# Kernel tuning notes

Hardware: AMD Instinct MI355X
Metric: run time of the kernel (lower is better)

## Reference

```python
import jax, jax.numpy as jnp
import numpy as np

HEADS = 4
DIM_HEAD = 32
SCALE = DIM_HEAD ** -0.5


def setup_inputs() -> dict:
    key = jax.random.key(0)
    k1, k2, k3 = jax.random.split(key, 3)
    B, C, H, W = 4, 128, 64, 64
    inner = HEADS * DIM_HEAD  # 128
    x = jax.random.normal(k1, (B, C, H, W), dtype=jnp.float32)
    # 1x1 conv weights == channel-mixing matrices [out_ch, in_ch]
    w_qkv = jax.random.normal(k2, (inner * 3, C), dtype=jnp.float32) * (C ** -0.5)
    w_proj = jax.random.normal(k3, (C, inner), dtype=jnp.float32) * (inner ** -0.5)
    b_proj = jnp.zeros((C,), dtype=jnp.float32)
    return {"x": x, "w_qkv": w_qkv, "w_proj": w_proj, "b_proj": b_proj}


def reference(x, w_qkv, w_proj, b_proj):
    b, c, h, w = x.shape
    n = h * w
    # 1x1 conv = per-pixel matmul over channels
    qkv = jnp.einsum('bchw,oc->bohw', x, w_qkv)  # [B, 3*inner, H, W]
    q, k, v = jnp.split(qkv, 3, axis=1)

    def to_heads(t):
        # [B, inner, H, W] -> [B, heads, HW, dim_head]
        return t.reshape(b, HEADS, DIM_HEAD, n).transpose(0, 1, 3, 2)

    q = to_heads(q) * SCALE
    k = to_heads(k)
    v = to_heads(v)
    # scores [B, heads, HW, HW]; softmax is max-stabilized (matches torch amax-subtract)
    scores = jnp.einsum('bhnd,bhmd->bhnm', q, k)
    attn = jax.nn.softmax(scores, axis=-1)
    out = jnp.einsum('bhnm,bhmd->bhnd', attn, v)  # [B, heads, HW, dim_head]
    out = out.transpose(0, 1, 3, 2).reshape(b, HEADS * DIM_HEAD, h, w)
    return jnp.einsum('bchw,oc->bohw', out, w_proj) + b_proj[None, :, None, None]
```

## Files before the change

kernel.cpp:

```cpp
#include <hip/hip_runtime.h>

typedef _Float16 f16;
typedef __attribute__((ext_vector_type(8))) f16 f16x8;
typedef __attribute__((ext_vector_type(4))) f16 f16x4;
typedef __attribute__((ext_vector_type(2))) __fp16 h16x2;
typedef __attribute__((ext_vector_type(4))) float floatx4;

#define NPIX 4096
#define KT   128
#define VROW 136

__global__ __launch_bounds__(256) void cvt_w(
    const float* __restrict__ wq, const float* __restrict__ wp,
    f16* __restrict__ wh, f16* __restrict__ wph)
{
    const int idx = (blockIdx.x * 256 + threadIdx.x) * 4;
    const float qs = 0.17677669529663687f * 1.4426950408889634f;
    float4 v;
    f16* dst;
    if (idx < 49152) { v = *(const float4*)(wq + idx); dst = wh + idx; }
    else             { v = *(const float4*)(wp + (idx - 49152)); dst = wph + (idx - 49152); }
    if (idx < 16384) { v.x *= qs; v.y *= qs; v.z *= qs; v.w *= qs; }
    h16x2 a = __builtin_amdgcn_cvt_pkrtz(v.x, v.y);
    h16x2 b = __builtin_amdgcn_cvt_pkrtz(v.z, v.w);
    f16x4 h; h[0] = (f16)a[0]; h[1] = (f16)a[1]; h[2] = (f16)b[0]; h[3] = (f16)b[1];
    *(f16x4*)dst = h;
}

__global__ __launch_bounds__(256) void qkv_mfma(
    const float* __restrict__ x, const f16* __restrict__ wh,
    f16* __restrict__ qh, f16* __restrict__ kh, f16* __restrict__ vth)
{
    const int tid  = threadIdx.x;
    const int wave = tid >> 6;
    const int lane = tid & 63;
    const int quad = lane >> 4;
    const int l16  = lane & 15;
    const int pbase = blockIdx.x * 64;
    const int b     = blockIdx.y;
    const int p_col = pbase + wave * 16 + l16;

    const float* xb = x + (size_t)b * 128 * NPIX;

    f16x8 xf[4];
#pragma unroll
    for (int kc = 0; kc < 4; ++kc) {
        const int c0 = kc * 32 + quad * 8;
        float e[8];
#pragma unroll
        for (int j = 0; j < 8; ++j)
            e[j] = xb[(size_t)(c0 + j) * NPIX + p_col];
#pragma unroll
        for (int j = 0; j < 4; ++j) {
            h16x2 pk = __builtin_amdgcn_cvt_pkrtz(e[2 * j], e[2 * j + 1]);
            xf[kc][2 * j] = (f16)pk[0]; xf[kc][2 * j + 1] = (f16)pk[1];
        }
    }

#pragma unroll
    for (int y = 0; y < 6; ++y) {
        floatx4 acc[4];
#pragma unroll
        for (int i = 0; i < 4; ++i) acc[i] = floatx4{0.f, 0.f, 0.f, 0.f};

        if (y < 4) {
#pragma unroll
            for (int n = 0; n < 4; ++n)
#pragma unroll
                for (int kc = 0; kc < 4; ++kc) {
                    f16x8 wf = *(const f16x8*)&wh[(size_t)(y * 64 + n * 16 + l16) * 128 + kc * 32 + quad * 8];
                    acc[n] = __builtin_amdgcn_mfma_f32_16x16x32_f16(xf[kc], wf, acc[n], 0, 0, 0);
                }
            f16* dst = (y < 2) ? qh : kh;
#pragma unroll
            for (int n = 0; n < 4; ++n) {
                const int og    = y * 64 + n * 16 + l16;
                const int local = og & 127;
                const int head  = local >> 5;
                const int d     = local & 31;
                f16* base = dst + (size_t)(b * 4 + head) * NPIX * 32;
#pragma unroll
                for (int r = 0; r < 4; ++r) {
                    const int p = pbase + wave * 16 + quad * 4 + r;
                    base[(size_t)p * 32 + d] = (f16)acc[n][r];
                }
            }
        } else {
#pragma unroll
            for (int m = 0; m < 4; ++m)
#pragma unroll
                for (int kc = 0; kc < 4; ++kc) {
                    f16x8 wf = *(const f16x8*)&wh[(size_t)(y * 64 + m * 16 + l16) * 128 + kc * 32 + quad * 8];
                    acc[m] = __builtin_amdgcn_mfma_f32_16x16x32_f16(wf, xf[kc], acc[m], 0, 0, 0);
                }
#pragma unroll
            for (int m = 0; m < 4; ++m)
#pragma unroll
                for (int r = 0; r < 4; ++r) {
                    const int ov   = (y - 4) * 64 + m * 16 + quad * 4 + r;
                    const int head = ov >> 5;
                    const int d    = ov & 31;
                    vth[((size_t)(b * 4 + head) * 32 + d) * NPIX + p_col] = (f16)acc[m][r];
                }
        }
    }
}

__global__ __launch_bounds__(256, 4) void attn_kernel(
    const f16* __restrict__ qh, const f16* __restrict__ kh,
    const f16* __restrict__ vth, f16* __restrict__ att)
{
    __shared__ f16 klds[KT * 32];
    __shared__ f16 vlds[32 * VROW];

    const int tid  = threadIdx.x;
    const int wave = tid >> 6;
    const int lane = tid & 63;
    const int quad = lane >> 4;
    const int l16  = lane & 15;

    const int n    = blockIdx.x;
    const int bh   = (n & 7) * 2 + ((n >> 3) & 1);
    const int qblk = n >> 4;
    const int qbase = qblk * 64 + wave * 16;

    const f16* kb = kh + (size_t)bh * NPIX * 32;
    const f16* vb = vth + (size_t)bh * 32 * NPIX;

    f16x8 qB = *(const f16x8*)(qh + ((size_t)bh * NPIX + qbase + l16) * 32 + quad * 8);

    floatx4 oacc[2];
    oacc[0] = floatx4{0.f, 0.f, 0.f, 0.f};
    oacc[1] = floatx4{0.f, 0.f, 0.f, 0.f};
    float lsum = 0.f;

    for (int kt = 0; kt < NPIX / KT; ++kt) {
        __syncthreads();
        {
            const int4* src = (const int4*)(kb + (size_t)kt * KT * 32);
            ((int4*)klds)[tid]       = src[tid];
            ((int4*)klds)[tid + 256] = src[tid + 256];
        }
        {
            const int r  = tid >> 3;
            const int cc = (tid & 7) * 2;
            const int4* vsrc = (const int4*)(vb + (size_t)r * NPIX + kt * KT + cc * 8);
            int4 v0 = vsrc[0], v1 = vsrc[1];
            int4* vdst = (int4*)(vlds + r * VROW + cc * 8);
            vdst[0] = v0; vdst[1] = v1;
        }
        __syncthreads();

        floatx4 st[8];
#pragma unroll
        for (int t = 0; t < 8; ++t) {
            f16x8 kf = *(const f16x8*)&klds[(t * 16 + l16) * 32 + quad * 8];
            floatx4 z = {0.f, 0.f, 0.f, 0.f};
            st[t] = __builtin_amdgcn_mfma_f32_16x16x32_f16(kf, qB, z, 0, 0, 0);
        }

        f16x4 paf[8];
#pragma unroll
        for (int t = 0; t < 8; ++t) {
            float e0 = __builtin_amdgcn_exp2f(st[t][0]);
            float e1 = __builtin_amdgcn_exp2f(st[t][1]);
            float e2 = __builtin_amdgcn_exp2f(st[t][2]);
            float e3 = __builtin_amdgcn_exp2f(st[t][3]);
            lsum += (e0 + e1) + (e2 + e3);
            h16x2 lo = __builtin_amdgcn_cvt_pkrtz(e0, e1);
            h16x2 hi = __builtin_amdgcn_cvt_pkrtz(e2, e3);
            paf[t][0] = (f16)lo[0]; paf[t][1] = (f16)lo[1];
            paf[t][2] = (f16)hi[0]; paf[t][3] = (f16)hi[1];
        }

#pragma unroll
        for (int g = 0; g < 4; ++g) {
            f16x8 pA;
#pragma unroll
            for (int j = 0; j < 4; ++j) { pA[j] = paf[2 * g][j]; pA[4 + j] = paf[2 * g + 1][j]; }
#pragma unroll
            for (int dh = 0; dh < 2; ++dh) {
                const f16* vrow = &vlds[(dh * 16 + l16) * VROW + 32 * g + quad * 4];
                f16x4 v0 = *(const f16x4*)(vrow);
                f16x4 v1 = *(const f16x4*)(vrow + 16);
                f16x8 vB;
#pragma unroll
                for (int j = 0; j < 4; ++j) { vB[j] = v0[j]; vB[4 + j] = v1[j]; }
                oacc[dh] = __builtin_amdgcn_mfma_f32_16x16x32_f16(pA, vB, oacc[dh], 0, 0, 0);
            }
        }
    }

    float l = lsum;
    l += __shfl_xor(l, 16);
    l += __shfl_xor(l, 32);
    const float inv = 1.0f / l;
#pragma unroll
    for (int r = 0; r < 4; ++r) {
        const float invr = __shfl(inv, quad * 4 + r);
        const int q = qbase + quad * 4 + r;
        f16* ob = att + ((size_t)bh * NPIX + q) * 32;
        ob[l16]      = (f16)(oacc[0][r] * invr);
        ob[16 + l16] = (f16)(oacc[1][r] * invr);
    }
}

__global__ __launch_bounds__(256) void proj_mfma(
    const f16* __restrict__ att, const f16* __restrict__ wph,
    const float* __restrict__ bp, float* __restrict__ out)
{
    const int tid  = threadIdx.x;
    const int wave = tid >> 6;
    const int lane = tid & 63;
    const int quad = lane >> 4;
    const int l16  = lane & 15;
    const int pbase = blockIdx.x * 64;
    const int b     = blockIdx.y;
    const int p_col = pbase + wave * 16 + l16;

    const f16* ab = att + (size_t)b * 4 * NPIX * 32;
    f16x8 bf[4];
#pragma unroll
    for (int kc = 0; kc < 4; ++kc)
        bf[kc] = *(const f16x8*)(ab + ((size_t)kc * NPIX + p_col) * 32 + quad * 8);

    floatx4 acc[8];
#pragma unroll
    for (int m = 0; m < 8; ++m) acc[m] = floatx4{0.f, 0.f, 0.f, 0.f};
#pragma unroll
    for (int m = 0; m < 8; ++m)
#pragma unroll
        for (int kc = 0; kc < 4; ++kc) {
            f16x8 af = *(const f16x8*)&wph[(size_t)(m * 16 + l16) * 128 + kc * 32 + quad * 8];
            acc[m] = __builtin_amdgcn_mfma_f32_16x16x32_f16(af, bf[kc], acc[m], 0, 0, 0);
        }

#pragma unroll
    for (int m = 0; m < 8; ++m)
#pragma unroll
        for (int r = 0; r < 4; ++r) {
            const int o = m * 16 + quad * 4 + r;
            out[((size_t)b * 128 + o) * NPIX + p_col] = acc[m][r] + bp[o];
        }
}

extern "C" void kernel_launch(void* const* d_in, const int* in_sizes, int n_in,
                              void* d_out, int out_size, void* d_ws, size_t ws_size,
                              hipStream_t stream)
{
    const float* x      = (const float*)d_in[0];
    const float* w_qkv  = (const float*)d_in[1];
    const float* w_proj = (const float*)d_in[2];
    const float* b_proj = (const float*)d_in[3];
    float* out = (float*)d_out;

    char* ws = (char*)d_ws;
    f16* qh  = (f16*)(ws);
    f16* kh  = (f16*)(ws + (4u << 20));
    f16* vth = (f16*)(ws + (8u << 20));
    f16* att = (f16*)(ws + (12u << 20));
    f16* wh  = (f16*)(ws + (16u << 20));
    f16* wph = (f16*)(ws + (16u << 20) + (96u << 10));

    cvt_w<<<dim3(64, 1, 1), 256, 0, stream>>>(w_qkv, w_proj, wh, wph);
    qkv_mfma<<<dim3(64, 4, 1), 256, 0, stream>>>(x, wh, qh, kh, vth);
    attn_kernel<<<dim3(1024, 1, 1), 256, 0, stream>>>(qh, kh, vth, att);
    proj_mfma<<<dim3(64, 4, 1), 256, 0, stream>>>(att, wph, b_proj, out);
}
```

Before: 153.0 us.

## Split attention over KV halves with combine pass; widen qkv and proj grids

The attention kernel now handles 128 queries per block, with two 16-row query tiles per wave, so each K/V tile loaded into LDS is reused twice. The KV range is split into two halves across blocks, which keeps the grid at 1024 blocks. Unnormalized partial outputs and row sums go to a workspace, and a new combine kernel merges them. The qkv and proj kernels gain a grid dimension over output-channel groups to raise parallelism. The cost is an extra launch and extra partial-output memory traffic, and the x loads in qkv are repeated across the six channel-group blocks.

```diff
diff --git a/kernel.cpp b/kernel.cpp
--- a/kernel.cpp
+++ b/kernel.cpp
@@ -37,7 +37,8 @@
     const int quad = lane >> 4;
     const int l16  = lane & 15;
     const int pbase = blockIdx.x * 64;
-    const int b     = blockIdx.y;
+    const int y     = blockIdx.y;
+    const int b     = blockIdx.z;
     const int p_col = pbase + wave * 16 + l16;
 
     const float* xb = x + (size_t)b * 128 * NPIX;
@@ -57,58 +58,55 @@
         }
     }
 
-#pragma unroll
-    for (int y = 0; y < 6; ++y) {
-        floatx4 acc[4];
-#pragma unroll
-        for (int i = 0; i < 4; ++i) acc[i] = floatx4{0.f, 0.f, 0.f, 0.f};
-
-        if (y < 4) {
-#pragma unroll
-            for (int n = 0; n < 4; ++n)
-#pragma unroll
-                for (int kc = 0; kc < 4; ++kc) {
-                    f16x8 wf = *(const f16x8*)&wh[(size_t)(y * 64 + n * 16 + l16) * 128 + kc * 32 + quad * 8];
-                    acc[n] = __builtin_amdgcn_mfma_f32_16x16x32_f16(xf[kc], wf, acc[n], 0, 0, 0);
-                }
-            f16* dst = (y < 2) ? qh : kh;
-#pragma unroll
-            for (int n = 0; n < 4; ++n) {
-                const int og    = y * 64 + n * 16 + l16;
-                const int local = og & 127;
-                const int head  = local >> 5;
-                const int d     = local & 31;
-                f16* base = dst + (size_t)(b * 4 + head) * NPIX * 32;
-#pragma unroll
-                for (int r = 0; r < 4; ++r) {
-                    const int p = pbase + wave * 16 + quad * 4 + r;
-                    base[(size_t)p * 32 + d] = (f16)acc[n][r];
-                }
-            }
-        } else {
-#pragma unroll
-            for (int m = 0; m < 4; ++m)
-#pragma unroll
-                for (int kc = 0; kc < 4; ++kc) {
-                    f16x8 wf = *(const f16x8*)&wh[(size_t)(y * 64 + m * 16 + l16) * 128 + kc * 32 + quad * 8];
-                    acc[m] = __builtin_amdgcn_mfma_f32_16x16x32_f16(wf, xf[kc], acc[m], 0, 0, 0);
-                }
-#pragma unroll
-            for (int m = 0; m < 4; ++m)
-#pragma unroll
-                for (int r = 0; r < 4; ++r) {
-                    const int ov   = (y - 4) * 64 + m * 16 + quad * 4 + r;
-                    const int head = ov >> 5;
-                    const int d    = ov & 31;
-                    vth[((size_t)(b * 4 + head) * 32 + d) * NPIX + p_col] = (f16)acc[m][r];
-                }
-        }
+    floatx4 acc[4];
+#pragma unroll
+    for (int i = 0; i < 4; ++i) acc[i] = floatx4{0.f, 0.f, 0.f, 0.f};
+
+    if (y < 4) {
+#pragma unroll
+        for (int n = 0; n < 4; ++n)
+#pragma unroll
+            for (int kc = 0; kc < 4; ++kc) {
+                f16x8 wf = *(const f16x8*)&wh[(size_t)(y * 64 + n * 16 + l16) * 128 + kc * 32 + quad * 8];
+                acc[n] = __builtin_amdgcn_mfma_f32_16x16x32_f16(xf[kc], wf, acc[n], 0, 0, 0);
+            }
+        f16* dst = (y < 2) ? qh : kh;
+#pragma unroll
+        for (int n = 0; n < 4; ++n) {
+            const int og    = y * 64 + n * 16 + l16;
+            const int local = og & 127;
+            const int head  = local >> 5;
+            const int d     = local & 31;
+            f16* base = dst + (size_t)(b * 4 + head) * NPIX * 32;
+#pragma unroll
+            for (int r = 0; r < 4; ++r) {
+                const int p = pbase + wave * 16 + quad * 4 + r;
+                base[(size_t)p * 32 + d] = (f16)acc[n][r];
+            }
+        }
+    } else {
+#pragma unroll
+        for (int m = 0; m < 4; ++m)
+#pragma unroll
+            for (int kc = 0; kc < 4; ++kc) {
+                f16x8 wf = *(const f16x8*)&wh[(size_t)(y * 64 + m * 16 + l16) * 128 + kc * 32 + quad * 8];
+                acc[m] = __builtin_amdgcn_mfma_f32_16x16x32_f16(wf, xf[kc], acc[m], 0, 0, 0);
+            }
+#pragma unroll
+        for (int m = 0; m < 4; ++m)
+#pragma unroll
+            for (int r = 0; r < 4; ++r) {
+                const int ov   = (y - 4) * 64 + m * 16 + quad * 4 + r;
+                const int head = ov >> 5;
+                const int d    = ov & 31;
+                vth[((size_t)(b * 4 + head) * 32 + d) * NPIX + p_col] = (f16)acc[m][r];
+            }
     }
 }
 
 __global__ __launch_bounds__(256, 4) void attn_kernel(
     const f16* __restrict__ qh, const f16* __restrict__ kh,
-    const f16* __restrict__ vth, f16* __restrict__ att)
+    const f16* __restrict__ vth, f16* __restrict__ po, float* __restrict__ pl)
 {
     __shared__ f16 klds[KT * 32];
     __shared__ f16 vlds[32 * VROW];
@@ -119,22 +117,28 @@
     const int quad = lane >> 4;
     const int l16  = lane & 15;
 
-    const int n    = blockIdx.x;
-    const int bh   = (n & 7) * 2 + ((n >> 3) & 1);
-    const int qblk = n >> 4;
-    const int qbase = qblk * 64 + wave * 16;
+    const int n     = blockIdx.x;
+    const int bh    = (n & 7) * 2 + ((n >> 3) & 1);
+    const int qblk  = (n >> 4) & 31;
+    const int split = n >> 9;
+    const int qbase = qblk * 128 + wave * 32;
 
     const f16* kb = kh + (size_t)bh * NPIX * 32;
     const f16* vb = vth + (size_t)bh * 32 * NPIX;
 
-    f16x8 qB = *(const f16x8*)(qh + ((size_t)bh * NPIX + qbase + l16) * 32 + quad * 8);
-
-    floatx4 oacc[2];
-    oacc[0] = floatx4{0.f, 0.f, 0.f, 0.f};
-    oacc[1] = floatx4{0.f, 0.f, 0.f, 0.f};
-    float lsum = 0.f;
-
-    for (int kt = 0; kt < NPIX / KT; ++kt) {
+    f16x8 qB[2];
+#pragma unroll
+    for (int h = 0; h < 2; ++h)
+        qB[h] = *(const f16x8*)(qh + ((size_t)bh * NPIX + qbase + h * 16 + l16) * 32 + quad * 8);
+
+    floatx4 oacc[2][2];
+#pragma unroll
+    for (int h = 0; h < 2; ++h)
+#pragma unroll
+        for (int dh = 0; dh < 2; ++dh) oacc[h][dh] = floatx4{0.f, 0.f, 0.f, 0.f};
+    float lsum[2] = {0.f, 0.f};
+
+    for (int kt = split * 16; kt < split * 16 + 16; ++kt) {
         __syncthreads();
         {
             const int4* src = (const int4*)(kb + (size_t)kt * KT * 32);
@@ -151,58 +155,87 @@
         }
         __syncthreads();
 
-        floatx4 st[8];
-#pragma unroll
-        for (int t = 0; t < 8; ++t) {
-            f16x8 kf = *(const f16x8*)&klds[(t * 16 + l16) * 32 + quad * 8];
-            floatx4 z = {0.f, 0.f, 0.f, 0.f};
-            st[t] = __builtin_amdgcn_mfma_f32_16x16x32_f16(kf, qB, z, 0, 0, 0);
-        }
-
-        f16x4 paf[8];
-#pragma unroll
-        for (int t = 0; t < 8; ++t) {
-            float e0 = __builtin_amdgcn_exp2f(st[t][0]);
-            float e1 = __builtin_amdgcn_exp2f(st[t][1]);
-            float e2 = __builtin_amdgcn_exp2f(st[t][2]);
-            float e3 = __builtin_amdgcn_exp2f(st[t][3]);
-            lsum += (e0 + e1) + (e2 + e3);
-            h16x2 lo = __builtin_amdgcn_cvt_pkrtz(e0, e1);
-            h16x2 hi = __builtin_amdgcn_cvt_pkrtz(e2, e3);
-            paf[t][0] = (f16)lo[0]; paf[t][1] = (f16)lo[1];
-            paf[t][2] = (f16)hi[0]; paf[t][3] = (f16)hi[1];
-        }
-
-#pragma unroll
-        for (int g = 0; g < 4; ++g) {
-            f16x8 pA;
-#pragma unroll
-            for (int j = 0; j < 4; ++j) { pA[j] = paf[2 * g][j]; pA[4 + j] = paf[2 * g + 1][j]; }
-#pragma unroll
-            for (int dh = 0; dh < 2; ++dh) {
-                const f16* vrow = &vlds[(dh * 16 + l16) * VROW + 32 * g + quad * 4];
-                f16x4 v0 = *(const f16x4*)(vrow);
-                f16x4 v1 = *(const f16x4*)(vrow + 16);
-                f16x8 vB;
-#pragma unroll
-                for (int j = 0; j < 4; ++j) { vB[j] = v0[j]; vB[4 + j] = v1[j]; }
-                oacc[dh] = __builtin_amdgcn_mfma_f32_16x16x32_f16(pA, vB, oacc[dh], 0, 0, 0);
+        f16x8 kf[8];
+#pragma unroll
+        for (int t = 0; t < 8; ++t)
+            kf[t] = *(const f16x8*)&klds[(t * 16 + l16) * 32 + quad * 8];
+
+#pragma unroll
+        for (int h = 0; h < 2; ++h) {
+            floatx4 st[8];
+#pragma unroll
+            for (int t = 0; t < 8; ++t) {
+                floatx4 z = {0.f, 0.f, 0.f, 0.f};
+                st[t] = __builtin_amdgcn_mfma_f32_16x16x32_f16(kf[t], qB[h], z, 0, 0, 0);
+            }
+            f16x4 paf[8];
+            float ls = 0.f;
+#pragma unroll
+            for (int t = 0; t < 8; ++t) {
+                float e0 = __builtin_amdgcn_exp2f(st[t][0]);
+                float e1 = __builtin_amdgcn_exp2f(st[t][1]);
+                float e2 = __builtin_amdgcn_exp2f(st[t][2]);
+                float e3 = __builtin_amdgcn_exp2f(st[t][3]);
+                ls += (e0 + e1) + (e2 + e3);
+                h16x2 lo = __builtin_amdgcn_cvt_pkrtz(e0, e1);
+                h16x2 hi = __builtin_amdgcn_cvt_pkrtz(e2, e3);
+                paf[t][0] = (f16)lo[0]; paf[t][1] = (f16)lo[1];
+                paf[t][2] = (f16)hi[0]; paf[t][3] = (f16)hi[1];
+            }
+            lsum[h] += ls;
+#pragma unroll
+            for (int g = 0; g < 4; ++g) {
+                f16x8 pA;
+#pragma unroll
+                for (int j = 0; j < 4; ++j) { pA[j] = paf[2 * g][j]; pA[4 + j] = paf[2 * g + 1][j]; }
+#pragma unroll
+                for (int dh = 0; dh < 2; ++dh) {
+                    const f16* vrow = &vlds[(dh * 16 + l16) * VROW + 32 * g + quad * 4];
+                    f16x4 v0 = *(const f16x4*)(vrow);
+                    f16x4 v1 = *(const f16x4*)(vrow + 16);
+                    f16x8 vB;
+#pragma unroll
+                    for (int j = 0; j < 4; ++j) { vB[j] = v0[j]; vB[4 + j] = v1[j]; }
+                    oacc[h][dh] = __builtin_amdgcn_mfma_f32_16x16x32_f16(pA, vB, oacc[h][dh], 0, 0, 0);
+                }
             }
         }
     }
 
-    float l = lsum;
-    l += __shfl_xor(l, 16);
-    l += __shfl_xor(l, 32);
-    const float inv = 1.0f / l;
-#pragma unroll
-    for (int r = 0; r < 4; ++r) {
-        const float invr = __shfl(inv, quad * 4 + r);
-        const int q = qbase + quad * 4 + r;
-        f16* ob = att + ((size_t)bh * NPIX + q) * 32;
-        ob[l16]      = (f16)(oacc[0][r] * invr);
-        ob[16 + l16] = (f16)(oacc[1][r] * invr);
+    const size_t bq = (size_t)(split * 16 + bh) * NPIX;
+#pragma unroll
+    for (int h = 0; h < 2; ++h) {
+        float l = lsum[h];
+        l += __shfl_xor(l, 16);
+        l += __shfl_xor(l, 32);
+        if (quad == 0)
+            pl[bq + qbase + h * 16 + l16] = l;
+        f16* poh = po + (bq + qbase + h * 16) * 32;
+#pragma unroll
+        for (int r = 0; r < 4; ++r) {
+            poh[(quad * 4 + r) * 32 + l16]      = (f16)oacc[h][0][r];
+            poh[(quad * 4 + r) * 32 + 16 + l16] = (f16)oacc[h][1][r];
+        }
     }
+}
+
+__global__ __launch_bounds__(256) void combine(
+    const f16* __restrict__ po, const float* __restrict__ pl,
+    f16* __restrict__ att)
+{
+    const int idx = blockIdx.x * 256 + threadIdx.x;
+    const int qg  = idx >> 2;
+    const int dg  = (idx & 3) * 8;
+    const size_t sstride = (size_t)16 * NPIX * 32;
+
+    f16x8 a = *(const f16x8*)(po + (size_t)qg * 32 + dg);
+    f16x8 b = *(const f16x8*)(po + sstride + (size_t)qg * 32 + dg);
+    const float inv = 1.0f / (pl[qg] + pl[qg + 16 * NPIX]);
+    f16x8 o;
+#pragma unroll
+    for (int j = 0; j < 8; ++j)
+        o[j] = (f16)(((float)a[j] + (float)b[j]) * inv);
+    *(f16x8*)(att + (size_t)qg * 32 + dg) = o;
 }
 
 __global__ __launch_bounds__(256) void proj_mfma(
@@ -215,7 +248,8 @@
     const int quad = lane >> 4;
     const int l16  = lane & 15;
     const int pbase = blockIdx.x * 64;
-    const int b     = blockIdx.y;
+    const int obase = blockIdx.y * 64;
+    const int b     = blockIdx.z;
     const int p_col = pbase + wave * 16 + l16;
 
     const f16* ab = att + (size_t)b * 4 * NPIX * 32;
@@ -224,22 +258,22 @@
     for (int kc = 0; kc < 4; ++kc)
         bf[kc] = *(const f16x8*)(ab + ((size_t)kc * NPIX + p_col) * 32 + quad * 8);
 
-    floatx4 acc[8];
-#pragma unroll
-    for (int m = 0; m < 8; ++m) acc[m] = floatx4{0.f, 0.f, 0.f, 0.f};
-#pragma unroll
-    for (int m = 0; m < 8; ++m)
+    floatx4 acc[4];
+#pragma unroll
+    for (int m = 0; m < 4; ++m) acc[m] = floatx4{0.f, 0.f, 0.f, 0.f};
+#pragma unroll
+    for (int m = 0; m < 4; ++m)
 #pragma unroll
         for (int kc = 0; kc < 4; ++kc) {
-            f16x8 af = *(const f16x8*)&wph[(size_t)(m * 16 + l16) * 128 + kc * 32 + quad * 8];
+            f16x8 af = *(const f16x8*)&wph[(size_t)(obase + m * 16 + l16) * 128 + kc * 32 + quad * 8];
             acc[m] = __builtin_amdgcn_mfma_f32_16x16x32_f16(af, bf[kc], acc[m], 0, 0, 0);
         }
 
 #pragma unroll
-    for (int m = 0; m < 8; ++m)
+    for (int m = 0; m < 4; ++m)
 #pragma unroll
         for (int r = 0; r < 4; ++r) {
-            const int o = m * 16 + quad * 4 + r;
+            const int o = obase + m * 16 + quad * 4 + r;
             out[((size_t)b * 128 + o) * NPIX + p_col] = acc[m][r] + bp[o];
         }
 }
@@ -255,15 +289,18 @@
     float* out = (float*)d_out;
 
     char* ws = (char*)d_ws;
-    f16* qh  = (f16*)(ws);
-    f16* kh  = (f16*)(ws + (4u << 20));
-    f16* vth = (f16*)(ws + (8u << 20));
-    f16* att = (f16*)(ws + (12u << 20));
-    f16* wh  = (f16*)(ws + (16u << 20));
-    f16* wph = (f16*)(ws + (16u << 20) + (96u << 10));
+    f16*   qh  = (f16*)(ws);
+    f16*   kh  = (f16*)(ws + (4u << 20));
+    f16*   vth = (f16*)(ws + (8u << 20));
+    f16*   att = (f16*)(ws + (12u << 20));
+    f16*   wh  = (f16*)(ws + (16u << 20));
+    f16*   wph = (f16*)(ws + (16u << 20) + (96u << 10));
+    float* pl  = (float*)(ws + (16u << 20) + (128u << 10));
+    f16*   po  = (f16*)(ws + (17u << 20));
 
     cvt_w<<<dim3(64, 1, 1), 256, 0, stream>>>(w_qkv, w_proj, wh, wph);
-    qkv_mfma<<<dim3(64, 4, 1), 256, 0, stream>>>(x, wh, qh, kh, vth);
-    attn_kernel<<<dim3(1024, 1, 1), 256, 0, stream>>>(qh, kh, vth, att);
-    proj_mfma<<<dim3(64, 4, 1), 256, 0, stream>>>(att, wph, b_proj, out);
-}
+    qkv_mfma<<<dim3(64, 6, 4), 256, 0, stream>>>(x, wh, qh, kh, vth);
+    attn_kernel<<<dim3(1024, 1, 1), 256, 0, stream>>>(qh, kh, vth, po, pl);
+    combine<<<dim3(1024, 1, 1), 256, 0, stream>>>(po, pl, att);
+    proj_mfma<<<dim3(64, 2, 4), 256, 0, stream>>>(att, wph, b_proj, out);
+}
```

New measurement: 141.5 us. 7.5% less time.
